# Kernel optimization log

Hardware: AMD Instinct MI355X
Metric: run time of the kernel (lower is better)

## Reference

```python
import jax, jax.numpy as jnp
import numpy as np

MASK_RATIO = 0.02
N2V_W, WAV_W, TV_W = 1.0, 0.2, 0.01
THRESHOLD = 50.0
LEVELS = 3


def setup_inputs() -> dict:
    key = jax.random.key(0)
    k1, k2, k3 = jax.random.split(key, 3)
    shape = (64, 1, 512, 512)
    pred = jax.random.uniform(k1, shape, dtype=jnp.float32)
    noisy_input = jax.random.uniform(k2, shape, dtype=jnp.float32)
    # N2V random blind-spot mask (torch.rand_like(pred) < mask_ratio)
    mask = jax.random.uniform(k3, shape, dtype=jnp.float32) < MASK_RATIO
    return {"pred": pred, "noisy_input": noisy_input, "mask": mask}


def haar_dwt2(x):
    # x: [B, H, W] with H, W even. Single-level 2D Haar DWT (pywt 'haar').
    a = x[:, 0::2, 0::2]
    b = x[:, 0::2, 1::2]
    c = x[:, 1::2, 0::2]
    d = x[:, 1::2, 1::2]
    ll = (a + b + c + d) * 0.5
    ch = (a + b - c - d) * 0.5  # horizontal detail
    cv = (a - b + c - d) * 0.5  # vertical detail
    cd = (a - b - c + d) * 0.5  # diagonal detail
    return ll, ch, cv, cd


def _level_l1(c, thr):
    # L1 between coeff and its (detached) soft-thresholded version
    target = jax.lax.stop_gradient(jnp.sign(c) * jnp.maximum(jnp.abs(c) - thr, 0.0))
    return jnp.mean(jnp.abs(c - target))


def reference(pred, noisy_input, mask):
    p = jnp.clip(pred, 0.0, 1.0)

    # --- Noise2Void masked L1 ---
    m = mask.astype(p.dtype)
    n2v = jnp.sum(jnp.abs(p - noisy_input) * m) / jnp.maximum(jnp.sum(m), 1.0)

    # --- Wavelet sparsity (multi-level Haar, soft-threshold targets) ---
    x = p[:, 0]  # [B, H, W]
    details = []  # finest first
    for _ in range(LEVELS):
        x, ch, cv, cd = haar_dwt2(x)
        details.append((ch, cv, cd))
    wav = jnp.asarray(0.0, dtype=p.dtype)
    for level_idx in range(1, LEVELS + 1):  # level_idx=1 -> coarsest (wavedec2 order)
        ch, cv, cd = details[LEVELS - level_idx]
        thr = (THRESHOLD / (2.0 ** (level_idx - 1))) / 255.0
        lvl = (_level_l1(ch, thr) + _level_l1(cv, thr) + _level_l1(cd, thr)) / 3.0
        wav = wav + (1.0 / level_idx) * lvl

    # --- Total variation ---
    tv = jnp.mean(jnp.abs(p[:, :, 1:, :] - p[:, :, :-1, :])) + \
         jnp.mean(jnp.abs(p[:, :, :, 1:] - p[:, :, :, :-1]))

    return N2V_W * n2v + WAV_W * wav + TV_W * tv
```

## Files before the change

### kernel.cpp

```cpp
#include <hip/hip_runtime.h>

#define NIMG 64
#define H 512
#define W 512

constexpr float THR_64  = 50.0f / 255.0f;
constexpr float THR_128 = 50.0f / 2.0f / 255.0f;
constexpr float THR_256 = 50.0f / 4.0f / 255.0f;

constexpr float SC_W1 = 0.2f  / 37748736.0f;
constexpr float SC_W2 = 0.2f  / 6291456.0f;
constexpr float SC_W3 = 0.2f  / 786432.0f;
constexpr float SC_TV = 0.01f / 16744448.0f;

__device__ __forceinline__ float wave_sum(float v) {
#pragma unroll
    for (int o = 32; o > 0; o >>= 1) v += __shfl_down(v, o, 64);
    return v;
}

__device__ __forceinline__ float clip01(float x) {
    return fminf(fmaxf(x, 0.0f), 1.0f);
}

__device__ __forceinline__ float4 clip4(float4 p) {
    p.x = clip01(p.x); p.y = clip01(p.y); p.z = clip01(p.z); p.w = clip01(p.w);
    return p;
}

__global__ __launch_bounds__(256) void kA(const float* __restrict__ pred,
                                          const float* __restrict__ noisy,
                                          const int* __restrict__ mask,
                                          float4* __restrict__ pA) {
    __shared__ float red[4][3];

    const int tid = threadIdx.x;
    const int lane = tid & 63;
    const int wv = tid >> 6;
    const int gw = (blockIdx.x << 2) + wv;
    const int n = gw >> 7;
    const int u = gw & 127;
    const int s = u >> 1;
    const int h = u & 1;
    const int r0 = s << 3;
    const int col0 = (h << 8) + (lane << 2);
    const size_t img = (size_t)n * (H * W);
    const size_t base = img + (size_t)r0 * W + col0;

    int4 m[8];
#pragma unroll
    for (int r = 0; r < 8; ++r)
        m[r] = *reinterpret_cast<const int4*>(mask + base + (size_t)r * W);

    float4 p[8];
#pragma unroll
    for (int r = 0; r < 8; ++r)
        p[r] = *reinterpret_cast<const float4*>(pred + base + (size_t)r * W);

    float4 hl = make_float4(0.f, 0.f, 0.f, 0.f);
    if (r0 > 0)
        hl = *reinterpret_cast<const float4*>(pred + base - W);

    float smv = 0.f;
    if (h == 0 && lane < 8)
        smv = pred[img + (size_t)(r0 + lane) * W + 256];

    float4 nz[8];
#pragma unroll
    for (int r = 0; r < 8; ++r) {
        nz[r] = make_float4(0.f, 0.f, 0.f, 0.f);
        if ((m[r].x | m[r].y | m[r].z | m[r].w) != 0)
            nz[r] = *reinterpret_cast<const float4*>(noisy + base + (size_t)r * W);
    }

#pragma unroll
    for (int r = 0; r < 8; ++r) p[r] = clip4(p[r]);
    hl = clip4(hl);
    smv = clip01(smv);

    float tv = 0.0f;
#pragma unroll
    for (int r = 0; r < 8; ++r) {
        const float4 q = p[r];
        tv += fabsf(q.y - q.x) + fabsf(q.z - q.y) + fabsf(q.w - q.z);
        float nb = __shfl_down(q.x, 1, 64);
        float seam_r = __shfl(smv, r, 64);
        if (lane == 63) nb = seam_r;
        if (lane < 63 || h == 0) tv += fabsf(nb - q.w);
    }
#pragma unroll
    for (int r = 0; r < 7; ++r) {
        tv += fabsf(p[r + 1].x - p[r].x) + fabsf(p[r + 1].y - p[r].y)
            + fabsf(p[r + 1].z - p[r].z) + fabsf(p[r + 1].w - p[r].w);
    }
    if (r0 > 0) {
        tv += fabsf(p[0].x - hl.x) + fabsf(p[0].y - hl.y)
            + fabsf(p[0].z - hl.z) + fabsf(p[0].w - hl.w);
    }

    float ll1[4][2];
    float wav1 = 0.0f;
#pragma unroll
    for (int rp = 0; rp < 4; ++rp) {
        const float4 t = p[2 * rp];
        const float4 bo = p[2 * rp + 1];
        float a, b, c, d, ch, cv, cd;
        a = t.x; b = t.y; c = bo.x; d = bo.y;
        ll1[rp][0] = (a + b + c + d) * 0.5f;
        ch = (a + b - c - d) * 0.5f; cv = (a - b + c - d) * 0.5f; cd = (a - b - c + d) * 0.5f;
        wav1 += fminf(fabsf(ch), THR_256) + fminf(fabsf(cv), THR_256) + fminf(fabsf(cd), THR_256);
        a = t.z; b = t.w; c = bo.z; d = bo.w;
        ll1[rp][1] = (a + b + c + d) * 0.5f;
        ch = (a + b - c - d) * 0.5f; cv = (a - b + c - d) * 0.5f; cd = (a - b - c + d) * 0.5f;
        wav1 += fminf(fabsf(ch), THR_256) + fminf(fabsf(cv), THR_256) + fminf(fabsf(cd), THR_256);
    }

    float ll2[2];
    float wav2 = 0.0f;
#pragma unroll
    for (int lp = 0; lp < 2; ++lp) {
        const float a = ll1[2 * lp][0], b = ll1[2 * lp][1];
        const float c = ll1[2 * lp + 1][0], d = ll1[2 * lp + 1][1];
        ll2[lp] = (a + b + c + d) * 0.5f;
        const float ch = (a + b - c - d) * 0.5f;
        const float cv = (a - b + c - d) * 0.5f;
        const float cd = (a - b - c + d) * 0.5f;
        wav2 += fminf(fabsf(ch), THR_128) + fminf(fabsf(cv), THR_128) + fminf(fabsf(cd), THR_128);
    }

    float w3 = 0.0f;
    {
        const float b3 = __shfl_xor(ll2[0], 1, 64);
        const float d3 = __shfl_xor(ll2[1], 1, 64);
        if ((lane & 1) == 0) {
            const float a = ll2[0], b = b3, c = ll2[1], d = d3;
            const float ch = (a + b - c - d) * 0.5f;
            const float cv = (a - b + c - d) * 0.5f;
            const float cd = (a - b - c + d) * 0.5f;
            w3 = fminf(fabsf(ch), THR_64) + fminf(fabsf(cv), THR_64)
               + fminf(fabsf(cd), THR_64);
        }
    }

    float n2v = 0.0f, msum = 0.0f;
#pragma unroll
    for (int r = 0; r < 8; ++r) {
        float mm;
        mm = m[r].x ? 1.f : 0.f; n2v += fabsf(p[r].x - nz[r].x) * mm; msum += mm;
        mm = m[r].y ? 1.f : 0.f; n2v += fabsf(p[r].y - nz[r].y) * mm; msum += mm;
        mm = m[r].z ? 1.f : 0.f; n2v += fabsf(p[r].z - nz[r].z) * mm; msum += mm;
        mm = m[r].w ? 1.f : 0.f; n2v += fabsf(p[r].w - nz[r].w) * mm; msum += mm;
    }

    const float comb = wav1 * SC_W1 + wav2 * SC_W2 + w3 * SC_W3 + tv * SC_TV;

    float v0 = wave_sum(n2v);
    float v1 = wave_sum(msum);
    float v2 = wave_sum(comb);
    if (lane == 0) {
        red[wv][0] = v0; red[wv][1] = v1; red[wv][2] = v2;
    }
    __syncthreads();
    if (tid == 0) {
        pA[blockIdx.x] = make_float4(red[0][0] + red[1][0] + red[2][0] + red[3][0],
                                     red[0][1] + red[1][1] + red[2][1] + red[3][1],
                                     red[0][2] + red[1][2] + red[2][2] + red[3][2],
                                     0.0f);
    }
}

__global__ __launch_bounds__(256) void kD(const float4* __restrict__ pA,
                                          float* __restrict__ out) {
    __shared__ float red[4][3];
    const int tid = threadIdx.x;
    const int lane = tid & 63, wv = tid >> 6;

    float s0 = 0, s1 = 0, s2 = 0;
#pragma unroll
    for (int j = 0; j < 8; ++j) {
        float4 v = pA[tid + (j << 8)];
        s0 += v.x; s1 += v.y; s2 += v.z;
    }
    s0 = wave_sum(s0); s1 = wave_sum(s1); s2 = wave_sum(s2);
    if (lane == 0) {
        red[wv][0] = s0; red[wv][1] = s1; red[wv][2] = s2;
    }
    __syncthreads();
    if (tid == 0) {
        float a0 = red[0][0] + red[1][0] + red[2][0] + red[3][0];
        float a1 = red[0][1] + red[1][1] + red[2][1] + red[3][1];
        float a2 = red[0][2] + red[1][2] + red[2][2] + red[3][2];
        out[0] = a0 / fmaxf(a1, 1.0f) + a2;
    }
}

extern "C" void kernel_launch(void* const* d_in, const int* in_sizes, int n_in,
                              void* d_out, int out_size, void* d_ws, size_t ws_size,
                              hipStream_t stream) {
    (void)in_sizes; (void)n_in; (void)out_size; (void)ws_size;
    const float* pred  = (const float*)d_in[0];
    const float* noisy = (const float*)d_in[1];
    const int*   mask  = (const int*)d_in[2];

    float4* pA = (float4*)d_ws;

    kA<<<2048, 256, 0, stream>>>(pred, noisy, mask, pA);
    kD<<<1, 256, 0, stream>>>(pA, (float*)d_out);
}
```

Measured before the change: 189.5 us.

## Process four tiles per wave with double-buffered register prefetch

```diff
diff --git a/kernel.cpp b/kernel.cpp
--- a/kernel.cpp
+++ b/kernel.cpp
@@ -3,6 +3,7 @@
 #define NIMG 64
 #define H 512
 #define W 512
+#define HW (H * W)
 
 constexpr float THR_64  = 50.0f / 255.0f;
 constexpr float THR_128 = 50.0f / 2.0f / 255.0f;
@@ -28,131 +29,161 @@
     return p;
 }
 
-__global__ __launch_bounds__(256) void kA(const float* __restrict__ pred,
-                                          const float* __restrict__ noisy,
-                                          const int* __restrict__ mask,
-                                          float4* __restrict__ pA) {
+
+#define TLOAD(PP, MM, HHL, SSM, TT)                                              \
+    {                                                                            \
+        const int u_ = (TT) & 127;                                               \
+        const int s_ = u_ >> 1, h_ = u_ & 1;                                     \
+        const int n_ = (TT) >> 7;                                                \
+        const int r0_ = s_ << 3;                                                 \
+        const size_t ib_ = (size_t)n_ * HW;                                      \
+        const size_t bb_ = ib_ + (size_t)r0_ * W + (h_ << 8) + (lane << 2);      \
+        _Pragma("unroll")                                                        \
+        for (int r = 0; r < 8; ++r)                                              \
+            MM[r] = *reinterpret_cast<const int4*>(mask + bb_ + (size_t)r * W);  \
+        _Pragma("unroll")                                                        \
+        for (int r = 0; r < 8; ++r)                                              \
+            PP[r] = *reinterpret_cast<const float4*>(pred + bb_ + (size_t)r * W);\
+        HHL = make_float4(0.f, 0.f, 0.f, 0.f);                                   \
+        if (r0_ > 0) HHL = *reinterpret_cast<const float4*>(pred + bb_ - W);     \
+        SSM = 0.f;                                                               \
+        if (h_ == 0 && lane < 8)                                                 \
+            SSM = pred[ib_ + (size_t)(r0_ + lane) * W + 256];                    \
+    }
+
+#define TNZ(MM, NZ, TT)                                                          \
+    {                                                                            \
+        const int u_ = (TT) & 127;                                               \
+        const int s_ = u_ >> 1, h_ = u_ & 1;                                     \
+        const int n_ = (TT) >> 7;                                                \
+        const size_t bb_ = (size_t)n_ * HW + (size_t)(s_ << 3) * W               \
+                         + (h_ << 8) + (lane << 2);                              \
+        _Pragma("unroll")                                                        \
+        for (int r = 0; r < 8; ++r) {                                            \
+            NZ[r] = make_float4(0.f, 0.f, 0.f, 0.f);                             \
+            if ((MM[r].x | MM[r].y | MM[r].z | MM[r].w) != 0)                    \
+                NZ[r] = *reinterpret_cast<const float4*>(noisy + bb_ + (size_t)r * W); \
+        }                                                                        \
+    }
+
+#define TCOMP(PP, MM, NZ, HHL, SSM, TT)                                          \
+    {                                                                            \
+        const int u_ = (TT) & 127;                                               \
+        const int s_ = u_ >> 1, h_ = u_ & 1;                                     \
+        const int r0_ = s_ << 3;                                                 \
+        _Pragma("unroll")                                                        \
+        for (int r = 0; r < 8; ++r) PP[r] = clip4(PP[r]);                        \
+        HHL = clip4(HHL);                                                        \
+        const float sm_ = clip01(SSM);                                           \
+        float tv = 0.0f;                                                         \
+        _Pragma("unroll")                                                        \
+        for (int r = 0; r < 8; ++r) {                                            \
+            const float4 q = PP[r];                                              \
+            tv += fabsf(q.y - q.x) + fabsf(q.z - q.y) + fabsf(q.w - q.z);        \
+            float nb = __shfl_down(q.x, 1, 64);                                  \
+            const float se = __shfl(sm_, r, 64);                                 \
+            if (lane == 63) nb = se;                                             \
+            if (lane < 63 || h_ == 0) tv += fabsf(nb - q.w);                     \
+        }                                                                        \
+        _Pragma("unroll")                                                        \
+        for (int r = 0; r < 7; ++r)                                              \
+            tv += fabsf(PP[r + 1].x - PP[r].x) + fabsf(PP[r + 1].y - PP[r].y)    \
+                + fabsf(PP[r + 1].z - PP[r].z) + fabsf(PP[r + 1].w - PP[r].w);   \
+        if (r0_ > 0)                                                             \
+            tv += fabsf(PP[0].x - HHL.x) + fabsf(PP[0].y - HHL.y)                \
+                + fabsf(PP[0].z - HHL.z) + fabsf(PP[0].w - HHL.w);               \
+        float ll1[4][2];                                                         \
+        float wav1 = 0.0f;                                                       \
+        _Pragma("unroll")                                                        \
+        for (int rp = 0; rp < 4; ++rp) {                                         \
+            const float4 t_ = PP[2 * rp];                                        \
+            const float4 bo = PP[2 * rp + 1];                                    \
+            float a, b, c, d, ch, cv, cd;                                        \
+            a = t_.x; b = t_.y; c = bo.x; d = bo.y;                              \
+            ll1[rp][0] = (a + b + c + d) * 0.5f;                                 \
+            ch = (a + b - c - d) * 0.5f; cv = (a - b + c - d) * 0.5f;            \
+            cd = (a - b - c + d) * 0.5f;                                         \
+            wav1 += fminf(fabsf(ch), THR_256) + fminf(fabsf(cv), THR_256)        \
+                  + fminf(fabsf(cd), THR_256);                                   \
+            a = t_.z; b = t_.w; c = bo.z; d = bo.w;                              \
+            ll1[rp][1] = (a + b + c + d) * 0.5f;                                 \
+            ch = (a + b - c - d) * 0.5f; cv = (a - b + c - d) * 0.5f;            \
+            cd = (a - b - c + d) * 0.5f;                                         \
+            wav1 += fminf(fabsf(ch), THR_256) + fminf(fabsf(cv), THR_256)        \
+                  + fminf(fabsf(cd), THR_256);                                   \
+        }                                                                        \
+        float ll2_[2];                                                           \
+        float wav2 = 0.0f;                                                       \
+        _Pragma("unroll")                                                        \
+        for (int lp = 0; lp < 2; ++lp) {                                         \
+            const float a = ll1[2 * lp][0], b = ll1[2 * lp][1];                  \
+            const float c = ll1[2 * lp + 1][0], d = ll1[2 * lp + 1][1];          \
+            ll2_[lp] = (a + b + c + d) * 0.5f;                                   \
+            const float ch = (a + b - c - d) * 0.5f;                             \
+            const float cv = (a - b + c - d) * 0.5f;                             \
+            const float cd = (a - b - c + d) * 0.5f;                             \
+            wav2 += fminf(fabsf(ch), THR_128) + fminf(fabsf(cv), THR_128)        \
+                  + fminf(fabsf(cd), THR_128);                                   \
+        }                                                                        \
+        float w3 = 0.0f;                                                         \
+        {                                                                        \
+            const float b3 = __shfl_xor(ll2_[0], 1, 64);                         \
+            const float d3 = __shfl_xor(ll2_[1], 1, 64);                         \
+            if ((lane & 1) == 0) {                                               \
+                const float a = ll2_[0], b = b3, c = ll2_[1], d = d3;            \
+                const float ch = (a + b - c - d) * 0.5f;                         \
+                const float cv = (a - b + c - d) * 0.5f;                         \
+                const float cd = (a - b - c + d) * 0.5f;                         \
+                w3 = fminf(fabsf(ch), THR_64) + fminf(fabsf(cv), THR_64)         \
+                   + fminf(fabsf(cd), THR_64);                                   \
+            }                                                                    \
+        }                                                                        \
+        _Pragma("unroll")                                                        \
+        for (int r = 0; r < 8; ++r) {                                            \
+            float mm;                                                            \
+            mm = MM[r].x ? 1.f : 0.f; n2v += fabsf(PP[r].x - NZ[r].x) * mm; msum += mm; \
+            mm = MM[r].y ? 1.f : 0.f; n2v += fabsf(PP[r].y - NZ[r].y) * mm; msum += mm; \
+            mm = MM[r].z ? 1.f : 0.f; n2v += fabsf(PP[r].z - NZ[r].z) * mm; msum += mm; \
+            mm = MM[r].w ? 1.f : 0.f; n2v += fabsf(PP[r].w - NZ[r].w) * mm; msum += mm; \
+        }                                                                        \
+        comb += wav1 * SC_W1 + wav2 * SC_W2 + w3 * SC_W3 + tv * SC_TV;           \
+    }
+
+__global__ __launch_bounds__(256, 2) void kA(const float* __restrict__ pred,
+                                             const float* __restrict__ noisy,
+                                             const int* __restrict__ mask,
+                                             float4* __restrict__ pOut) {
     __shared__ float red[4][3];
 
     const int tid = threadIdx.x;
     const int lane = tid & 63;
     const int wv = tid >> 6;
     const int gw = (blockIdx.x << 2) + wv;
-    const int n = gw >> 7;
-    const int u = gw & 127;
-    const int s = u >> 1;
-    const int h = u & 1;
-    const int r0 = s << 3;
-    const int col0 = (h << 8) + (lane << 2);
-    const size_t img = (size_t)n * (H * W);
-    const size_t base = img + (size_t)r0 * W + col0;
-
-    int4 m[8];
-#pragma unroll
-    for (int r = 0; r < 8; ++r)
-        m[r] = *reinterpret_cast<const int4*>(mask + base + (size_t)r * W);
-
-    float4 p[8];
-#pragma unroll
-    for (int r = 0; r < 8; ++r)
-        p[r] = *reinterpret_cast<const float4*>(pred + base + (size_t)r * W);
-
-    float4 hl = make_float4(0.f, 0.f, 0.f, 0.f);
-    if (r0 > 0)
-        hl = *reinterpret_cast<const float4*>(pred + base - W);
-
-    float smv = 0.f;
-    if (h == 0 && lane < 8)
-        smv = pred[img + (size_t)(r0 + lane) * W + 256];
-
-    float4 nz[8];
-#pragma unroll
-    for (int r = 0; r < 8; ++r) {
-        nz[r] = make_float4(0.f, 0.f, 0.f, 0.f);
-        if ((m[r].x | m[r].y | m[r].z | m[r].w) != 0)
-            nz[r] = *reinterpret_cast<const float4*>(noisy + base + (size_t)r * W);
-    }
-
-#pragma unroll
-    for (int r = 0; r < 8; ++r) p[r] = clip4(p[r]);
-    hl = clip4(hl);
-    smv = clip01(smv);
-
-    float tv = 0.0f;
-#pragma unroll
-    for (int r = 0; r < 8; ++r) {
-        const float4 q = p[r];
-        tv += fabsf(q.y - q.x) + fabsf(q.z - q.y) + fabsf(q.w - q.z);
-        float nb = __shfl_down(q.x, 1, 64);
-        float seam_r = __shfl(smv, r, 64);
-        if (lane == 63) nb = seam_r;
-        if (lane < 63 || h == 0) tv += fabsf(nb - q.w);
-    }
-#pragma unroll
-    for (int r = 0; r < 7; ++r) {
-        tv += fabsf(p[r + 1].x - p[r].x) + fabsf(p[r + 1].y - p[r].y)
-            + fabsf(p[r + 1].z - p[r].z) + fabsf(p[r + 1].w - p[r].w);
-    }
-    if (r0 > 0) {
-        tv += fabsf(p[0].x - hl.x) + fabsf(p[0].y - hl.y)
-            + fabsf(p[0].z - hl.z) + fabsf(p[0].w - hl.w);
-    }
-
-    float ll1[4][2];
-    float wav1 = 0.0f;
-#pragma unroll
-    for (int rp = 0; rp < 4; ++rp) {
-        const float4 t = p[2 * rp];
-        const float4 bo = p[2 * rp + 1];
-        float a, b, c, d, ch, cv, cd;
-        a = t.x; b = t.y; c = bo.x; d = bo.y;
-        ll1[rp][0] = (a + b + c + d) * 0.5f;
-        ch = (a + b - c - d) * 0.5f; cv = (a - b + c - d) * 0.5f; cd = (a - b - c + d) * 0.5f;
-        wav1 += fminf(fabsf(ch), THR_256) + fminf(fabsf(cv), THR_256) + fminf(fabsf(cd), THR_256);
-        a = t.z; b = t.w; c = bo.z; d = bo.w;
-        ll1[rp][1] = (a + b + c + d) * 0.5f;
-        ch = (a + b - c - d) * 0.5f; cv = (a - b + c - d) * 0.5f; cd = (a - b - c + d) * 0.5f;
-        wav1 += fminf(fabsf(ch), THR_256) + fminf(fabsf(cv), THR_256) + fminf(fabsf(cd), THR_256);
-    }
-
-    float ll2[2];
-    float wav2 = 0.0f;
-#pragma unroll
-    for (int lp = 0; lp < 2; ++lp) {
-        const float a = ll1[2 * lp][0], b = ll1[2 * lp][1];
-        const float c = ll1[2 * lp + 1][0], d = ll1[2 * lp + 1][1];
-        ll2[lp] = (a + b + c + d) * 0.5f;
-        const float ch = (a + b - c - d) * 0.5f;
-        const float cv = (a - b + c - d) * 0.5f;
-        const float cd = (a - b - c + d) * 0.5f;
-        wav2 += fminf(fabsf(ch), THR_128) + fminf(fabsf(cv), THR_128) + fminf(fabsf(cd), THR_128);
-    }
-
-    float w3 = 0.0f;
-    {
-        const float b3 = __shfl_xor(ll2[0], 1, 64);
-        const float d3 = __shfl_xor(ll2[1], 1, 64);
-        if ((lane & 1) == 0) {
-            const float a = ll2[0], b = b3, c = ll2[1], d = d3;
-            const float ch = (a + b - c - d) * 0.5f;
-            const float cv = (a - b + c - d) * 0.5f;
-            const float cd = (a - b - c + d) * 0.5f;
-            w3 = fminf(fabsf(ch), THR_64) + fminf(fabsf(cv), THR_64)
-               + fminf(fabsf(cd), THR_64);
-        }
-    }
-
-    float n2v = 0.0f, msum = 0.0f;
-#pragma unroll
-    for (int r = 0; r < 8; ++r) {
-        float mm;
-        mm = m[r].x ? 1.f : 0.f; n2v += fabsf(p[r].x - nz[r].x) * mm; msum += mm;
-        mm = m[r].y ? 1.f : 0.f; n2v += fabsf(p[r].y - nz[r].y) * mm; msum += mm;
-        mm = m[r].z ? 1.f : 0.f; n2v += fabsf(p[r].z - nz[r].z) * mm; msum += mm;
-        mm = m[r].w ? 1.f : 0.f; n2v += fabsf(p[r].w - nz[r].w) * mm; msum += mm;
-    }
-
-    const float comb = wav1 * SC_W1 + wav2 * SC_W2 + w3 * SC_W3 + tv * SC_TV;
+    const int t0 = gw << 2;
+
+    float4 pA_[8], pB_[8];
+    int4   mA_[8], mB_[8];
+    float4 hA_, hB_;
+    float  sA_, sB_;
+    float4 nz_[8];
+    float n2v = 0.0f, msum = 0.0f, comb = 0.0f;
+
+    TLOAD(pA_, mA_, hA_, sA_, t0)
+
+    TLOAD(pB_, mB_, hB_, sB_, t0 + 1)
+    TNZ(mA_, nz_, t0)
+    TCOMP(pA_, mA_, nz_, hA_, sA_, t0)
+
+    TLOAD(pA_, mA_, hA_, sA_, t0 + 2)
+    TNZ(mB_, nz_, t0 + 1)
+    TCOMP(pB_, mB_, nz_, hB_, sB_, t0 + 1)
+
+    TLOAD(pB_, mB_, hB_, sB_, t0 + 3)
+    TNZ(mA_, nz_, t0 + 2)
+    TCOMP(pA_, mA_, nz_, hA_, sA_, t0 + 2)
+
+    TNZ(mB_, nz_, t0 + 3)
+    TCOMP(pB_, mB_, nz_, hB_, sB_, t0 + 3)
 
     float v0 = wave_sum(n2v);
     float v1 = wave_sum(msum);
@@ -162,10 +193,10 @@
     }
     __syncthreads();
     if (tid == 0) {
-        pA[blockIdx.x] = make_float4(red[0][0] + red[1][0] + red[2][0] + red[3][0],
-                                     red[0][1] + red[1][1] + red[2][1] + red[3][1],
-                                     red[0][2] + red[1][2] + red[2][2] + red[3][2],
-                                     0.0f);
+        pOut[blockIdx.x] = make_float4(red[0][0] + red[1][0] + red[2][0] + red[3][0],
+                                       red[0][1] + red[1][1] + red[2][1] + red[3][1],
+                                       red[0][2] + red[1][2] + red[2][2] + red[3][2],
+                                       0.0f);
     }
 }
 
@@ -177,7 +208,7 @@
 
     float s0 = 0, s1 = 0, s2 = 0;
 #pragma unroll
-    for (int j = 0; j < 8; ++j) {
+    for (int j = 0; j < 2; ++j) {
         float4 v = pA[tid + (j << 8)];
         s0 += v.x; s1 += v.y; s2 += v.z;
     }
@@ -204,6 +235,6 @@
 
     float4* pA = (float4*)d_ws;
 
-    kA<<<2048, 256, 0, stream>>>(pred, noisy, mask, pA);
+    kA<<<512, 256, 0, stream>>>(pred, noisy, mask, pA);
     kD<<<1, 256, 0, stream>>>(pA, (float*)d_out);
 }
```

After: 260.3 us. +37.4%, slower.

## Use nontemporal loads, 128-thread blocks, and per-wave partials without block sync

Applied to the files above, without the earlier changes.

```diff
diff --git a/kernel.cpp b/kernel.cpp
--- a/kernel.cpp
+++ b/kernel.cpp
@@ -3,6 +3,10 @@
 #define NIMG 64
 #define H 512
 #define W 512
+#define HW (H * W)
+
+typedef float f4 __attribute__((ext_vector_type(4)));
+typedef int   i4 __attribute__((ext_vector_type(4)));
 
 constexpr float THR_64  = 50.0f / 255.0f;
 constexpr float THR_128 = 50.0f / 2.0f / 255.0f;
@@ -23,54 +27,59 @@
     return fminf(fmaxf(x, 0.0f), 1.0f);
 }
 
-__device__ __forceinline__ float4 clip4(float4 p) {
+__device__ __forceinline__ f4 clip4(f4 p) {
     p.x = clip01(p.x); p.y = clip01(p.y); p.z = clip01(p.z); p.w = clip01(p.w);
     return p;
 }
 
-__global__ __launch_bounds__(256) void kA(const float* __restrict__ pred,
+__device__ __forceinline__ f4 ntl4(const float* p) {
+    return __builtin_nontemporal_load(reinterpret_cast<const f4*>(p));
+}
+__device__ __forceinline__ i4 ntli(const int* p) {
+    return __builtin_nontemporal_load(reinterpret_cast<const i4*>(p));
+}
+
+__global__ __launch_bounds__(128) void kA(const float* __restrict__ pred,
                                           const float* __restrict__ noisy,
                                           const int* __restrict__ mask,
-                                          float4* __restrict__ pA) {
-    __shared__ float red[4][3];
-
+                                          f4* __restrict__ pOut) {
     const int tid = threadIdx.x;
     const int lane = tid & 63;
     const int wv = tid >> 6;
-    const int gw = (blockIdx.x << 2) + wv;
+    const int gw = (blockIdx.x << 1) + wv;
     const int n = gw >> 7;
     const int u = gw & 127;
     const int s = u >> 1;
     const int h = u & 1;
     const int r0 = s << 3;
     const int col0 = (h << 8) + (lane << 2);
-    const size_t img = (size_t)n * (H * W);
+    const size_t img = (size_t)n * HW;
     const size_t base = img + (size_t)r0 * W + col0;
 
-    int4 m[8];
+    i4 m[8];
 #pragma unroll
     for (int r = 0; r < 8; ++r)
-        m[r] = *reinterpret_cast<const int4*>(mask + base + (size_t)r * W);
-
-    float4 p[8];
+        m[r] = ntli(mask + base + (size_t)r * W);
+
+    f4 p[8];
 #pragma unroll
     for (int r = 0; r < 8; ++r)
-        p[r] = *reinterpret_cast<const float4*>(pred + base + (size_t)r * W);
-
-    float4 hl = make_float4(0.f, 0.f, 0.f, 0.f);
+        p[r] = ntl4(pred + base + (size_t)r * W);
+
+    f4 hl = {0.f, 0.f, 0.f, 0.f};
     if (r0 > 0)
-        hl = *reinterpret_cast<const float4*>(pred + base - W);
+        hl = ntl4(pred + base - W);
 
     float smv = 0.f;
     if (h == 0 && lane < 8)
         smv = pred[img + (size_t)(r0 + lane) * W + 256];
 
-    float4 nz[8];
+    f4 nz[8];
 #pragma unroll
     for (int r = 0; r < 8; ++r) {
-        nz[r] = make_float4(0.f, 0.f, 0.f, 0.f);
+        nz[r] = (f4){0.f, 0.f, 0.f, 0.f};
         if ((m[r].x | m[r].y | m[r].z | m[r].w) != 0)
-            nz[r] = *reinterpret_cast<const float4*>(noisy + base + (size_t)r * W);
+            nz[r] = ntl4(noisy + base + (size_t)r * W);
     }
 
 #pragma unroll
@@ -81,7 +90,7 @@
     float tv = 0.0f;
 #pragma unroll
     for (int r = 0; r < 8; ++r) {
-        const float4 q = p[r];
+        const f4 q = p[r];
         tv += fabsf(q.y - q.x) + fabsf(q.z - q.y) + fabsf(q.w - q.z);
         float nb = __shfl_down(q.x, 1, 64);
         float seam_r = __shfl(smv, r, 64);
@@ -102,8 +111,8 @@
     float wav1 = 0.0f;
 #pragma unroll
     for (int rp = 0; rp < 4; ++rp) {
-        const float4 t = p[2 * rp];
-        const float4 bo = p[2 * rp + 1];
+        const f4 t = p[2 * rp];
+        const f4 bo = p[2 * rp + 1];
         float a, b, c, d, ch, cv, cd;
         a = t.x; b = t.y; c = bo.x; d = bo.y;
         ll1[rp][0] = (a + b + c + d) * 0.5f;
@@ -158,18 +167,12 @@
     float v1 = wave_sum(msum);
     float v2 = wave_sum(comb);
     if (lane == 0) {
-        red[wv][0] = v0; red[wv][1] = v1; red[wv][2] = v2;
-    }
-    __syncthreads();
-    if (tid == 0) {
-        pA[blockIdx.x] = make_float4(red[0][0] + red[1][0] + red[2][0] + red[3][0],
-                                     red[0][1] + red[1][1] + red[2][1] + red[3][1],
-                                     red[0][2] + red[1][2] + red[2][2] + red[3][2],
-                                     0.0f);
-    }
-}
-
-__global__ __launch_bounds__(256) void kD(const float4* __restrict__ pA,
+        f4 o = {v0, v1, v2, 0.f};
+        pOut[gw] = o;
+    }
+}
+
+__global__ __launch_bounds__(256) void kD(const f4* __restrict__ pA,
                                           float* __restrict__ out) {
     __shared__ float red[4][3];
     const int tid = threadIdx.x;
@@ -177,8 +180,8 @@
 
     float s0 = 0, s1 = 0, s2 = 0;
 #pragma unroll
-    for (int j = 0; j < 8; ++j) {
-        float4 v = pA[tid + (j << 8)];
+    for (int j = 0; j < 32; ++j) {
+        f4 v = pA[tid + (j << 8)];
         s0 += v.x; s1 += v.y; s2 += v.z;
     }
     s0 = wave_sum(s0); s1 = wave_sum(s1); s2 = wave_sum(s2);
@@ -202,8 +205,8 @@
     const float* noisy = (const float*)d_in[1];
     const int*   mask  = (const int*)d_in[2];
 
-    float4* pA = (float4*)d_ws;
-
-    kA<<<2048, 256, 0, stream>>>(pred, noisy, mask, pA);
+    f4* pA = (f4*)d_ws;
+
+    kA<<<4096, 128, 0, stream>>>(pred, noisy, mask, pA);
     kD<<<1, 256, 0, stream>>>(pA, (float*)d_out);
 }
```

Result: no change. 192.5 us (+1.6%).
